# Kernel optimization log

Hardware: AMD Instinct MI355X
Metric: run time of the kernel (lower is better)

Reference implementation:

```python
import jax, jax.numpy as jnp
import numpy as np

NEG_SLOPE = 0.2  # PyG GATConv default leaky_relu slope
NUM_GRAPHS = 64


def gat_layer(x, src, dst, W, a_src, a_dst, b, heads, out_ch, concat, N):
    # x: [N, in_ch] -> h: [N, H, C]
    h = (x @ W).reshape(N, heads, out_ch)
    a_s = jnp.einsum('nhc,hc->nh', h, a_src)  # [N, H]
    a_d = jnp.einsum('nhc,hc->nh', h, a_dst)  # [N, H]
    e = jax.nn.leaky_relu(a_s[src] + a_d[dst], NEG_SLOPE)  # [E, H]
    # segment softmax over edges grouped by destination node
    emax = jax.ops.segment_max(e, dst, num_segments=N)
    emax = jnp.where(jnp.isfinite(emax), emax, 0.0)
    ex = jnp.exp(e - emax[dst])
    denom = jax.ops.segment_sum(ex, dst, num_segments=N)
    alpha = ex / (denom[dst] + 1e-16)  # [E, H]
    out = jax.ops.segment_sum(alpha[:, :, None] * h[src], dst, num_segments=N)  # [N, H, C]
    out = out.reshape(N, heads * out_ch) if concat else out.mean(axis=1)
    return out + b


def setup_inputs() -> dict:
    key = jax.random.key(0)
    ks = jax.random.split(key, 16)
    N, E, F_IN, H, C, NC = 50000, 800000, 128, 4, 64, 200
    x = jax.random.normal(ks[0], (N, F_IN), dtype=jnp.float32)
    edge_index = jax.random.randint(ks[1], (2, E), 0, N, dtype=jnp.int32)
    batch = jnp.sort(jax.random.randint(ks[2], (N,), 0, NUM_GRAPHS, dtype=jnp.int32))
    s = 0.05
    params = dict(
        W1=jax.random.normal(ks[3], (F_IN, H * C), jnp.float32) * s,
        a_src1=jax.random.normal(ks[4], (H, C), jnp.float32) * s,
        a_dst1=jax.random.normal(ks[5], (H, C), jnp.float32) * s,
        b1=jnp.zeros((H * C,), jnp.float32),
        W2=jax.random.normal(ks[6], (H * C, H * C), jnp.float32) * s,
        a_src2=jax.random.normal(ks[7], (H, C), jnp.float32) * s,
        a_dst2=jax.random.normal(ks[8], (H, C), jnp.float32) * s,
        b2=jnp.zeros((H * C,), jnp.float32),
        W3=jax.random.normal(ks[9], (H * C, C), jnp.float32) * s,
        a_src3=jax.random.normal(ks[10], (1, C), jnp.float32) * s,
        a_dst3=jax.random.normal(ks[11], (1, C), jnp.float32) * s,
        b3=jnp.zeros((C,), jnp.float32),
        Wc=jax.random.normal(ks[12], (C, NC), jnp.float32) * s,
        bc=jnp.zeros((NC,), jnp.float32),
    )
    return dict(x=x, edge_index=edge_index, batch=batch, **params)


def reference(x, edge_index, batch,
              W1, a_src1, a_dst1, b1,
              W2, a_src2, a_dst2, b2,
              W3, a_src3, a_dst3, b3,
              Wc, bc):
    N = x.shape[0]
    # PyG GATConv adds self-loops by default
    loop = jnp.arange(N, dtype=edge_index.dtype)
    src = jnp.concatenate([edge_index[0], loop])
    dst = jnp.concatenate([edge_index[1], loop])
    H, C = a_src1.shape
    h = gat_layer(x, src, dst, W1, a_src1, a_dst1, b1, H, C, True, N)
    h = jax.nn.elu(h)  # dropout is identity in eval mode
    h = gat_layer(h, src, dst, W2, a_src2, a_dst2, b2, H, C, True, N)
    h = jax.nn.elu(h)
    h = gat_layer(h, src, dst, W3, a_src3, a_dst3, b3, 1, C, False, N)
    h = jax.nn.elu(h)
    # global mean pool per graph
    sums = jax.ops.segment_sum(h, batch, num_segments=NUM_GRAPHS)
    counts = jax.ops.segment_sum(jnp.ones((N,), h.dtype), batch, num_segments=NUM_GRAPHS)
    pooled = sums / jnp.maximum(counts, 1.0)[:, None]
    return pooled @ Wc + bc
```

## Files before the change

### kernel.cpp

```cpp
#include <hip/hip_runtime.h>


typedef __attribute__((ext_vector_type(8))) __bf16 bf16x8;
typedef __attribute__((ext_vector_type(4))) float f32x4;
typedef __attribute__((ext_vector_type(8))) unsigned short u16x8;
typedef __attribute__((ext_vector_type(4))) unsigned short u16x4;

#define LOG2E 1.44269504f

static __device__ __forceinline__ unsigned short f2bf(float f) {
    unsigned u = __float_as_uint(f);
    unsigned r = (u + 0x7fffu + ((u >> 16) & 1u)) >> 16;
    return (unsigned short)r;
}
static __device__ __forceinline__ float bf2f(unsigned short s) {
    return __uint_as_float(((unsigned)s) << 16);
}

static __device__ __forceinline__ void g2lds16(const unsigned short* g,
                                               unsigned short* l) {
    __builtin_amdgcn_global_load_lds(
        (const __attribute__((address_space(1))) unsigned int*)g,
        (__attribute__((address_space(3))) unsigned int*)l, 16, 0, 0);
}

__global__ void count_edges(const int* __restrict__ ei, int* __restrict__ deg,
                            int* __restrict__ epos, int E) {
    int i = blockIdx.x * blockDim.x + threadIdx.x;
    if (i >= E) return;
    int dst = ei[E + i];
    epos[i] = atomicAdd(&deg[dst], 1);
}

__global__ __launch_bounds__(256) void scan_partial(const int* __restrict__ deg,
                                                    int* __restrict__ rowptr,
                                                    int* __restrict__ blockSums, int N) {
    int t = threadIdx.x;
    int lane = t & 63, wv = t >> 6;
    int base = blockIdx.x * 1024 + t * 4;
    int v[4];
#pragma unroll
    for (int j = 0; j < 4; ++j) v[j] = (base + j < N) ? deg[base + j] + 1 : 0;
    int local = v[0] + v[1] + v[2] + v[3];
    int x = local;
#pragma unroll
    for (int off = 1; off < 64; off <<= 1) {
        int y = __shfl_up(x, off);
        if (lane >= off) x += y;
    }
    __shared__ int wsum[4];
    if (lane == 63) wsum[wv] = x;
    __syncthreads();
    int woff = 0;
    for (int i = 0; i < wv; ++i) woff += wsum[i];
    int run = woff + x - local;
#pragma unroll
    for (int j = 0; j < 4; ++j) {
        if (base + j < N) rowptr[base + j] = run;
        run += v[j];
    }
    if (t == 255) blockSums[blockIdx.x] = woff + x;
}

__global__ void scan_blocks(int* __restrict__ blockSums, int* __restrict__ rowptr,
                            int NB, int N) {
    int lane = threadIdx.x;
    int carry = 0;
    for (int b0 = 0; b0 < NB; b0 += 64) {
        int i = b0 + lane;
        int v = (i < NB) ? blockSums[i] : 0;
        int x = v;
#pragma unroll
        for (int off = 1; off < 64; off <<= 1) {
            int y = __shfl_up(x, off);
            if (lane >= off) x += y;
        }
        if (i < NB) blockSums[i] = carry + x - v;
        carry += __shfl(x, 63);
    }
    if (lane == 0) {
        int c = N >> 10;
        int offN;
        if (c < NB) {
            offN = blockSums[c];
        } else {
            blockSums[c] = 0;
            offN = 0;
        }
        rowptr[N] = carry - offN;
    }
}

__global__ void scatter_edges(const int* __restrict__ ei, const int* __restrict__ rowptr,
                              const int* __restrict__ bs,
                              const int* __restrict__ deg, const int* __restrict__ epos,
                              int* __restrict__ srcs, int E, int N) {
    int i = blockIdx.x * blockDim.x + threadIdx.x;
    int tot = E + N;
    if (i >= tot) return;
    if (i < E) {
        int dst = ei[E + i];
        srcs[rowptr[dst] + bs[dst >> 10] + epos[i]] = ei[i];
    } else {
        int d = i - E;
        srcs[rowptr[d] + bs[d >> 10] + deg[d]] = d;
    }
}

__global__ void prep_cast(const float* __restrict__ W1, unsigned short* __restrict__ Wt1,
                          const float* __restrict__ W2, unsigned short* __restrict__ Wt2,
                          const float* __restrict__ W3, unsigned short* __restrict__ Wt3,
                          int n1, int n2, int n3, int F_IN, int HC, int C) {
    int i = blockIdx.x * blockDim.x + threadIdx.x;
    if (i < n1) {
        int n = i / F_IN, k = i - n * F_IN;
        Wt1[i] = f2bf(W1[(size_t)k * HC + n]);
        return;
    }
    i -= n1;
    if (i < n2) {
        int n = i / HC, k = i - n * HC;
        Wt2[i] = f2bf(W2[(size_t)k * HC + n]);
        return;
    }
    i -= n2;
    if (i < n3) {
        int n = i / HC, k = i - n * HC;
        Wt3[i] = f2bf(W3[(size_t)k * C + n]);
    }
}

#define BK 32

template <bool AF32, int WAVES_N>
__global__ __launch_bounds__(256) void gemm_bf16(const void* __restrict__ Av,
                                                 const unsigned short* __restrict__ Bt,
                                                 unsigned short* __restrict__ C,
                                                 const float* __restrict__ a_src,
                                                 const float* __restrict__ a_dst,
                                                 float* __restrict__ as_o,
                                                 float* __restrict__ ad_o,
                                                 int M, int N, int K, int H) {
    constexpr int BMt = (4 / WAVES_N) * 64;
    constexpr int BNt = WAVES_N * 64;
    constexpr int ASLOTS = BMt * 4;
    constexpr int ROUNDS = (BMt + BNt) / 64;
    __shared__ unsigned short As[BMt * BK];
    __shared__ unsigned short Bs[BNt * BK];
    int t = threadIdx.x;
    int bm = blockIdx.y * BMt;
    int wave = t >> 6, lane = t & 63;
    int wm = (wave / WAVES_N) * 64, wn = (wave % WAVES_N) * 64;
    int quad = lane >> 4, mr = lane & 15;

    f32x4 zero = {0.f, 0.f, 0.f, 0.f};
    f32x4 acc[4][4];
#pragma unroll
    for (int i = 0; i < 4; ++i)
#pragma unroll
        for (int j = 0; j < 4; ++j) acc[i][j] = zero;

    int sw = quad ^ ((mr >> 1) & 3);
    int aoff[4], boff[4];
#pragma unroll
    for (int i = 0; i < 4; ++i) {
        aoff[i] = (wm + i * 16 + mr) * BK + sw * 8;
        boff[i] = (wn + i * 16 + mr) * BK + sw * 8;
    }

    for (int k0 = 0; k0 < K; k0 += BK) {
        ushort4 ua0, ua1;
        if (AF32) {
            int slot = t;
            int row = slot >> 2;
            int sg = (slot & 3) ^ ((row >> 1) & 3);
            int gra = bm + row;
            float4 lo = make_float4(0.f, 0.f, 0.f, 0.f), hi = lo;
            if (gra < M) {
                const float* Af = (const float*)Av;
                lo = *(const float4*)&Af[(size_t)gra * K + k0 + sg * 8];
                hi = *(const float4*)&Af[(size_t)gra * K + k0 + sg * 8 + 4];
            }
            ua0 = make_ushort4(f2bf(lo.x), f2bf(lo.y), f2bf(lo.z), f2bf(lo.w));
            ua1 = make_ushort4(f2bf(hi.x), f2bf(hi.y), f2bf(hi.z), f2bf(hi.w));
        }
        __syncthreads();
        if (AF32) {
            int slot = t;
            *(ushort4*)&As[slot * 8]     = ua0;
            *(ushort4*)&As[slot * 8 + 4] = ua1;
#pragma unroll
            for (int r = 0; r < BNt / 64; ++r) {
                int slotw = r * 256 + wave * 64;
                int bslot = slotw + lane;
                int row = bslot >> 2;
                int sg = (bslot & 3) ^ ((row >> 1) & 3);
                g2lds16(&Bt[(size_t)row * K + k0 + sg * 8], &Bs[slotw * 8]);
            }
        } else {
            const unsigned short* Ab = (const unsigned short*)Av;
#pragma unroll
            for (int r = 0; r < ROUNDS; ++r) {
                int slotw = r * 256 + wave * 64;
                int slot = slotw + lane;
                if (slotw < ASLOTS) {
                    int row = slot >> 2;
                    int sg = (slot & 3) ^ ((row >> 1) & 3);
                    int gra = bm + row;
                    if (gra < M)
                        g2lds16(&Ab[(size_t)gra * K + k0 + sg * 8], &As[slotw * 8]);
                } else {
                    int bslot = slot - ASLOTS;
                    int row = bslot >> 2;
                    int sg = (bslot & 3) ^ ((row >> 1) & 3);
                    g2lds16(&Bt[(size_t)row * K + k0 + sg * 8], &Bs[(slotw - ASLOTS) * 8]);
                }
            }
        }
        __syncthreads();

        bf16x8 af[4], bfr[4];
#pragma unroll
        for (int i = 0; i < 4; ++i) {
            af[i]  = *(bf16x8*)&As[aoff[i]];
            bfr[i] = *(bf16x8*)&Bs[boff[i]];
        }
#pragma unroll
        for (int i = 0; i < 4; ++i)
#pragma unroll
            for (int j = 0; j < 4; ++j)
                acc[i][j] = __builtin_amdgcn_mfma_f32_16x16x32_bf16(af[i], bfr[j], acc[i][j], 0, 0, 0);
    }

    {
        int head = wn >> 6;
        float asv[4], adv[4];
#pragma unroll
        for (int j = 0; j < 4; ++j) {
            asv[j] = a_src[head * 64 + j * 16 + mr];
            adv[j] = a_dst[head * 64 + j * 16 + mr];
        }
#pragma unroll
        for (int i = 0; i < 4; ++i) {
#pragma unroll
            for (int r = 0; r < 4; ++r) {
                float ps = acc[i][0][r] * asv[0] + acc[i][1][r] * asv[1]
                         + acc[i][2][r] * asv[2] + acc[i][3][r] * asv[3];
                float pd = acc[i][0][r] * adv[0] + acc[i][1][r] * adv[1]
                         + acc[i][2][r] * adv[2] + acc[i][3][r] * adv[3];
#pragma unroll
                for (int off2 = 1; off2 < 16; off2 <<= 1) {
                    ps += __shfl_xor(ps, off2);
                    pd += __shfl_xor(pd, off2);
                }
                int grow = bm + wm + i * 16 + quad * 4 + r;
                if (mr == 0 && grow < M) {
                    as_o[(size_t)grow * H + head] = ps * LOG2E;
                    ad_o[(size_t)grow * H + head] = pd * LOG2E;
                }
            }
        }
    }

#pragma unroll
    for (int i = 0; i < 4; ++i) {
#pragma unroll
        for (int r = 0; r < 4; ++r) {
            int grow = bm + wm + i * 16 + quad * 4 + r;
            if (grow >= M) continue;
#pragma unroll
            for (int j = 0; j < 4; ++j) {
                int gcol = wn + j * 16 + mr;
                C[(size_t)grow * N + gcol] = f2bf(acc[i][j][r]);
            }
        }
    }
}

template <int H, int NPW, int VPL, bool OUTF32>
__global__ __launch_bounds__(256) void gat_aggregate(const unsigned short* __restrict__ hbuf,
                                                     const float* __restrict__ as_i,
                                                     const float* __restrict__ ad_i,
                                                     const int* __restrict__ rowptr,
                                                     const int* __restrict__ bs,
                                                     const int* __restrict__ srcs,
                                                     const float* __restrict__ bias,
                                                     void* __restrict__ out_v, int N) {
    constexpr int LPN = 64 / NPW;
    constexpr int HC = LPN * VPL;
    int wid = (blockIdx.x * blockDim.x + threadIdx.x) >> 6;
    int lane = threadIdx.x & 63;
    int sub = lane / LPN;
    int li  = lane % LPN;
    int node = wid * NPW + sub;
    if (node >= N) return;
    int row = rowptr[node] + bs[node >> 10];
    int end = rowptr[node + 1] + bs[(node + 1) >> 10];
    int len = end - row;
    const int hd_lane = (li * VPL) >> 6;

    float advh = ad_i[(size_t)node * H + hd_lane];

    float acc[VPL];
#pragma unroll
    for (int j = 0; j < VPL; ++j) acc[j] = 0.f;
    float l = 0.f;

    const int U = 4;
    for (int base = 0; base < len; base += U) {
        int s[U];
        float cf[U];
#pragma unroll
        for (int u = 0; u < U; ++u) {
            int idx = base + u;
            int ii = row + ((idx < len) ? idx : (len - 1));
            s[u] = srcs[ii];
        }
#pragma unroll
        for (int u = 0; u < U; ++u) cf[u] = as_i[(size_t)s[u] * H + hd_lane];
        if (VPL == 8) {
            u16x8 r[U];
#pragma unroll
            for (int u = 0; u < U; ++u)
                r[u] = *(const u16x8*)&hbuf[(size_t)s[u] * HC + li * VPL];
#pragma unroll
            for (int u = 0; u < U; ++u) {
                float e = cf[u] + advh;
                e = fmaxf(e, 0.2f * e);
                float wgt = (base + u < len) ? exp2f(e) : 0.f;
                l += wgt;
#pragma unroll
                for (int j = 0; j < 8; ++j) acc[j] += wgt * bf2f(r[u][j]);
            }
        } else {
            u16x4 r[U];
#pragma unroll
            for (int u = 0; u < U; ++u)
                r[u] = *(const u16x4*)&hbuf[(size_t)s[u] * HC + li * VPL];
#pragma unroll
            for (int u = 0; u < U; ++u) {
                float e = cf[u] + advh;
                e = fmaxf(e, 0.2f * e);
                float wgt = (base + u < len) ? exp2f(e) : 0.f;
                l += wgt;
#pragma unroll
                for (int j = 0; j < VPL; ++j) acc[j] += wgt * bf2f(r[u][j]);
            }
        }
    }

    float inv_l = 1.f / (l + 1e-16f);
    float vals[VPL];
#pragma unroll
    for (int j = 0; j < VPL; ++j) {
        float v = acc[j] * inv_l + bias[li * VPL + j];
        vals[j] = (v > 0.f) ? v : (__expf(v) - 1.f);
    }
    if (OUTF32) {
        float* out = (float*)out_v;
        if (VPL == 4) {
            float4 o = make_float4(vals[0], vals[1], vals[2], vals[3]);
            *(float4*)&out[(size_t)node * HC + li * 4] = o;
        } else {
#pragma unroll
            for (int j = 0; j < VPL; ++j)
                out[(size_t)node * HC + li * VPL + j] = vals[j];
        }
    } else {
        unsigned short* out = (unsigned short*)out_v;
        if (VPL == 8) {
            u16x8 o;
#pragma unroll
            for (int j = 0; j < 8; ++j) o[j] = f2bf(vals[j]);
            *(u16x8*)&out[(size_t)node * HC + li * 8] = o;
        } else {
            ushort4 o;
            o.x = f2bf(vals[0]); o.y = f2bf(vals[1]);
            o.z = f2bf(vals[2]); o.w = f2bf(vals[3]);
            *(ushort4*)&out[(size_t)node * HC + li * 4] = o;
        }
    }
}

#define POOL_CHUNK 128
__global__ __launch_bounds__(256) void pool_kernel(const float* __restrict__ hf,
                                                   const int* __restrict__ batch,
                                                   float* __restrict__ sums,
                                                   float* __restrict__ counts, int N) {
    int t = threadIdx.x;
    int c = t & 63, sub = t >> 6;
    int start = blockIdx.x * POOL_CHUNK;
    int end = min(start + POOL_CHUNK, N);
    float acc = 0.f, cnt = 0.f;
    int cur = -1;
    for (int n = start + sub; n < end; n += 4) {
        int g = batch[n];
        if (g != cur) {
            if (cur >= 0) {
                atomicAdd(&sums[cur * 64 + c], acc);
                if (c == 0) atomicAdd(&counts[cur], cnt);
            }
            cur = g; acc = 0.f; cnt = 0.f;
        }
        acc += hf[(size_t)n * 64 + c];
        cnt += 1.f;
    }
    if (cur >= 0) {
        atomicAdd(&sums[cur * 64 + c], acc);
        if (c == 0) atomicAdd(&counts[cur], cnt);
    }
}

__global__ void classify(const float* __restrict__ sums, const float* __restrict__ counts,
                         const float* __restrict__ Wc, const float* __restrict__ bc,
                         float* __restrict__ out, int NC) {
    __shared__ float p[64];
    int g = blockIdx.x;
    if (threadIdx.x < 64) {
        float cnt = fmaxf(counts[g], 1.0f);
        p[threadIdx.x] = sums[g * 64 + threadIdx.x] / cnt;
    }
    __syncthreads();
    int k = threadIdx.x;
    if (k < NC) {
        float acc = bc[k];
        for (int c = 0; c < 64; ++c) acc += p[c] * Wc[c * NC + k];
        out[g * NC + k] = acc;
    }
}

static inline size_t align_up(size_t x, size_t a) { return (x + a - 1) / a * a; }

extern "C" void kernel_launch(void* const* d_in, const int* in_sizes, int n_in,
                              void* d_out, int out_size, void* d_ws, size_t ws_size,
                              hipStream_t stream) {
    const float* x      = (const float*)d_in[0];
    const int*   ei     = (const int*)d_in[1];
    const int*   batch  = (const int*)d_in[2];
    const float* W1     = (const float*)d_in[3];
    const float* a_src1 = (const float*)d_in[4];
    const float* a_dst1 = (const float*)d_in[5];
    const float* b1     = (const float*)d_in[6];
    const float* W2     = (const float*)d_in[7];
    const float* a_src2 = (const float*)d_in[8];
    const float* a_dst2 = (const float*)d_in[9];
    const float* b2     = (const float*)d_in[10];
    const float* W3     = (const float*)d_in[11];
    const float* a_src3 = (const float*)d_in[12];
    const float* a_dst3 = (const float*)d_in[13];
    const float* b3     = (const float*)d_in[14];
    const float* Wc     = (const float*)d_in[15];
    const float* bc     = (const float*)d_in[16];

    const int N    = in_sizes[2];
    const int E    = in_sizes[1] / 2;
    const int F_IN = in_sizes[0] / N;
    const int HC   = in_sizes[6];
    const int C    = in_sizes[14];
    const int NC   = in_sizes[16];
    const int Etot = E + N;
    const int NB   = (N + 1023) / 1024;
    const int NPB  = (N + POOL_CHUNK - 1) / POOL_CHUNK;

    char* w = (char*)d_ws;
    size_t off = 0;
    auto alloc = [&](size_t bytes) -> void* {
        void* p = w + off;
        off = align_up(off + bytes, 256);
        return p;
    };
    int*   deg    = (int*)alloc((size_t)N * 4);
    float* sums   = (float*)alloc((size_t)(64 * 64 + 64) * 4);
    float* counts = sums + 64 * 64;
    int*   rowptr = (int*)alloc((size_t)(N + 1) * 4);
    int*   epos   = (int*)alloc((size_t)E * 4);
    int*   srcs   = (int*)alloc((size_t)Etot * 4);
    int*   bsums  = (int*)alloc((size_t)(NB + 1) * 4);
    float* as_buf = (float*)alloc((size_t)N * 4 * 4);
    float* ad_buf = (float*)alloc((size_t)N * 4 * 4);
    unsigned short* Wt1 = (unsigned short*)alloc((size_t)HC * F_IN * 2);
    unsigned short* Wt2 = (unsigned short*)alloc((size_t)HC * HC * 2);
    unsigned short* Wt3 = (unsigned short*)alloc((size_t)C * HC * 2);
    unsigned short* hA  = (unsigned short*)alloc((size_t)N * HC * 2);
    unsigned short* hB  = (unsigned short*)alloc((size_t)N * HC * 2);
    unsigned short* hC  = (unsigned short*)alloc((size_t)N * C * 2);
    float* bufF   = (float*)alloc((size_t)N * C * 4);

    const int TPB = 256;

    hipMemsetAsync(deg, 0, (char*)(sums + 64 * 64 + 64) - (char*)deg, stream);

    count_edges<<<(E + TPB - 1) / TPB, TPB, 0, stream>>>(ei, deg, epos, E);
    scan_partial<<<NB, 256, 0, stream>>>(deg, rowptr, bsums, N);
    scan_blocks<<<1, 64, 0, stream>>>(bsums, rowptr, NB, N);
    scatter_edges<<<(Etot + TPB - 1) / TPB, TPB, 0, stream>>>(ei, rowptr, bsums, deg, epos, srcs, E, N);

    int n1 = HC * F_IN, n2 = HC * HC, n3 = C * HC;
    int ntot = n1 + n2 + n3;
    prep_cast<<<(ntot + TPB - 1) / TPB, TPB, 0, stream>>>(
        W1, Wt1, W2, Wt2, W3, Wt3, n1, n2, n3, F_IN, HC, C);

    dim3 gWide(1, (N + 63) / 64);
    dim3 gNarrow(1, (N + 255) / 256);
    int aggBlocks12 = (((N + 1) / 2) + 3) / 4;
    int aggBlocks3  = (((N + 3) / 4) + 3) / 4;

    gemm_bf16<true, 4><<<gWide, 256, 0, stream>>>(x, Wt1, hA, a_src1, a_dst1, as_buf, ad_buf, N, HC, F_IN, 4);
    gat_aggregate<4, 2, 8, false><<<aggBlocks12, 256, 0, stream>>>(hA, as_buf, ad_buf, rowptr, bsums, srcs, b1, hB, N);

    gemm_bf16<false, 4><<<gWide, 256, 0, stream>>>(hB, Wt2, hA, a_src2, a_dst2, as_buf, ad_buf, N, HC, HC, 4);
    gat_aggregate<4, 2, 8, false><<<aggBlocks12, 256, 0, stream>>>(hA, as_buf, ad_buf, rowptr, bsums, srcs, b2, hB, N);

    gemm_bf16<false, 1><<<gNarrow, 256, 0, stream>>>(hB, Wt3, hC, a_src3, a_dst3, as_buf, ad_buf, N, C, HC, 1);
    gat_aggregate<1, 4, 4, true><<<aggBlocks3, 256, 0, stream>>>(hC, as_buf, ad_buf, rowptr, bsums, srcs, b3, bufF, N);

    pool_kernel<<<NPB, 256, 0, stream>>>(bufF, batch, sums, counts, N);
    classify<<<64, 256, 0, stream>>>(sums, counts, Wc, bc, (float*)d_out, NC);
}
```

Baseline: 399.8 us.

## Cooperatively load edge indices and double-buffer gathers in GAT aggregation

Each lane now loads one source index per chunk of LPN edges, and the indices are spread across the node's lanes with shuffles, so serial scalar index loads are no longer needed. The gather loop is software-pipelined with two register buffers: the next group of attention scalars and feature vectors is issued before the current group is accumulated, which hides memory latency. This raises register pressure and may issue extra clamped or wasted loads past the end of each chunk.

```diff
diff --git a/kernel.cpp b/kernel.cpp
--- a/kernel.cpp
+++ b/kernel.cpp
@@ -277,6 +277,10 @@
     }
 }
 
+template <int VPL> struct VecT;
+template <> struct VecT<8> { using T = u16x8; };
+template <> struct VecT<4> { using T = u16x4; };
+
 template <int H, int NPW, int VPL, bool OUTF32>
 __global__ __launch_bounds__(256) void gat_aggregate(const unsigned short* __restrict__ hbuf,
                                                      const float* __restrict__ as_i,
@@ -288,6 +292,8 @@
                                                      void* __restrict__ out_v, int N) {
     constexpr int LPN = 64 / NPW;
     constexpr int HC = LPN * VPL;
+    constexpr int U = 4;
+    using vload = typename VecT<VPL>::T;
     int wid = (blockIdx.x * blockDim.x + threadIdx.x) >> 6;
     int lane = threadIdx.x & 63;
     int sub = lane / LPN;
@@ -298,55 +304,70 @@
     int end = rowptr[node + 1] + bs[(node + 1) >> 10];
     int len = end - row;
     const int hd_lane = (li * VPL) >> 6;
+    const int subbase = sub * LPN;
 
     float advh = ad_i[(size_t)node * H + hd_lane];
+    const unsigned short* hb_l = hbuf + li * VPL;
 
     float acc[VPL];
 #pragma unroll
     for (int j = 0; j < VPL; ++j) acc[j] = 0.f;
     float l = 0.f;
 
-    const int U = 4;
-    for (int base = 0; base < len; base += U) {
-        int s[U];
-        float cf[U];
-#pragma unroll
-        for (int u = 0; u < U; ++u) {
-            int idx = base + u;
-            int ii = row + ((idx < len) ? idx : (len - 1));
-            s[u] = srcs[ii];
-        }
-#pragma unroll
-        for (int u = 0; u < U; ++u) cf[u] = as_i[(size_t)s[u] * H + hd_lane];
-        if (VPL == 8) {
-            u16x8 r[U];
-#pragma unroll
-            for (int u = 0; u < U; ++u)
-                r[u] = *(const u16x8*)&hbuf[(size_t)s[u] * HC + li * VPL];
-#pragma unroll
-            for (int u = 0; u < U; ++u) {
-                float e = cf[u] + advh;
-                e = fmaxf(e, 0.2f * e);
-                float wgt = (base + u < len) ? exp2f(e) : 0.f;
-                l += wgt;
-#pragma unroll
-                for (int j = 0; j < 8; ++j) acc[j] += wgt * bf2f(r[u][j]);
-            }
-        } else {
-            u16x4 r[U];
-#pragma unroll
-            for (int u = 0; u < U; ++u)
-                r[u] = *(const u16x4*)&hbuf[(size_t)s[u] * HC + li * VPL];
-#pragma unroll
-            for (int u = 0; u < U; ++u) {
-                float e = cf[u] + advh;
-                e = fmaxf(e, 0.2f * e);
-                float wgt = (base + u < len) ? exp2f(e) : 0.f;
-                l += wgt;
-#pragma unroll
-                for (int j = 0; j < VPL; ++j) acc[j] += wgt * bf2f(r[u][j]);
-            }
-        }
+    for (int c0 = 0; c0 < len; c0 += LPN) {
+        int cend = len - c0; cend = (cend < LPN) ? cend : LPN;
+        if (cend <= 0) break;
+        int ei_ = c0 + li; ei_ = (ei_ < len) ? ei_ : (len - 1);
+        int svec = srcs[row + ei_];
+
+        int sA[U], sB[U];
+        float cfA[U], cfB[U];
+        vload rA[U], rB[U];
+
+#define AGG_ISSUE(sX, cfX, rX, b0)                                          \
+        do {                                                                \
+            _Pragma("unroll")                                               \
+            for (int u = 0; u < U; ++u) {                                   \
+                int idx = (b0) + u;                                         \
+                idx = (idx < cend) ? idx : (cend - 1);                      \
+                sX[u] = __shfl(svec, subbase + idx);                        \
+            }                                                               \
+            _Pragma("unroll")                                               \
+            for (int u = 0; u < U; ++u)                                     \
+                cfX[u] = as_i[(size_t)sX[u] * H + hd_lane];                 \
+            _Pragma("unroll")                                               \
+            for (int u = 0; u < U; ++u)                                     \
+                rX[u] = *(const vload*)&hb_l[(size_t)sX[u] * HC];           \
+        } while (0)
+
+#define AGG_COMPUTE(cfX, rX, b0)                                            \
+        do {                                                                \
+            _Pragma("unroll")                                               \
+            for (int u = 0; u < U; ++u) {                                   \
+                float e = cfX[u] + advh;                                    \
+                e = fmaxf(e, 0.2f * e);                                     \
+                float wgt = ((b0) + u < cend) ? exp2f(e) : 0.f;             \
+                l += wgt;                                                   \
+                _Pragma("unroll")                                           \
+                for (int j = 0; j < VPL; ++j)                               \
+                    acc[j] += wgt * bf2f(rX[u][j]);                         \
+            }                                                               \
+        } while (0)
+
+        AGG_ISSUE(sA, cfA, rA, 0);
+        int b = 0;
+        while (true) {
+            AGG_ISSUE(sB, cfB, rB, b + U);
+            AGG_COMPUTE(cfA, rA, b);
+            b += U;
+            if (b >= cend) break;
+            AGG_ISSUE(sA, cfA, rA, b + U);
+            AGG_COMPUTE(cfB, rB, b);
+            b += U;
+            if (b >= cend) break;
+        }
+#undef AGG_ISSUE
+#undef AGG_COMPUTE
     }
 
     float inv_l = 1.f / (l + 1e-16f);
```

Result: no change. 406.3 us (+1.6%).

## Fold attention vectors into weights, double-buffer GEMM LDS, unroll aggregation more

Applied to the files above, without the earlier changes.

Precomputes W·a_src and W·a_dst as an extra 16-column bf16 matrix so the attention logits come from an extra MFMA per k-step instead of a shuffle reduction in the epilogue. Double-buffers the A/B/W LDS tiles so global loads for the next k-tile overlap the MFMAs on the current one, at the cost of doubled shared memory. Raises the edge unroll in the aggregation kernel from 4 to 8 for more memory-level parallelism. The attention logits now use bf16-rounded folded weights, which changes precision slightly.

```diff
diff --git a/kernel.cpp b/kernel.cpp
--- a/kernel.cpp
+++ b/kernel.cpp
@@ -4,7 +4,6 @@
 typedef __attribute__((ext_vector_type(8))) __bf16 bf16x8;
 typedef __attribute__((ext_vector_type(4))) float f32x4;
 typedef __attribute__((ext_vector_type(8))) unsigned short u16x8;
-typedef __attribute__((ext_vector_type(4))) unsigned short u16x4;
 
 #define LOG2E 1.44269504f
 
@@ -130,14 +129,61 @@
     }
 }
 
+__global__ void prep_asd(const float* __restrict__ W1, const float* __restrict__ as1,
+                         const float* __restrict__ ad1,
+                         const float* __restrict__ W2, const float* __restrict__ as2,
+                         const float* __restrict__ ad2,
+                         const float* __restrict__ W3, const float* __restrict__ as3,
+                         const float* __restrict__ ad3,
+                         unsigned short* __restrict__ wasd1,
+                         unsigned short* __restrict__ wasd2,
+                         unsigned short* __restrict__ wasd3) {
+    int i = blockIdx.x * blockDim.x + threadIdx.x;
+    if (i < 16 * 128) {
+        int p = i >> 7, k = i & 127;
+        float v = 0.f;
+        if (p < 8) {
+            const float* a = (p < 4) ? as1 : ad1;
+            int hh = p & 3;
+            for (int c = 0; c < 64; ++c)
+                v += W1[(size_t)k * 256 + hh * 64 + c] * a[hh * 64 + c];
+        }
+        wasd1[i] = f2bf(v);
+        return;
+    }
+    i -= 16 * 128;
+    if (i < 16 * 256) {
+        int p = i >> 8, k = i & 255;
+        float v = 0.f;
+        if (p < 8) {
+            const float* a = (p < 4) ? as2 : ad2;
+            int hh = p & 3;
+            for (int c = 0; c < 64; ++c)
+                v += W2[(size_t)k * 256 + hh * 64 + c] * a[hh * 64 + c];
+        }
+        wasd2[i] = f2bf(v);
+        return;
+    }
+    i -= 16 * 256;
+    if (i < 16 * 256) {
+        int p = i >> 8, k = i & 255;
+        float v = 0.f;
+        if (p < 2) {
+            const float* a = p ? ad3 : as3;
+            for (int c = 0; c < 64; ++c)
+                v += W3[(size_t)k * 64 + c] * a[c];
+        }
+        wasd3[i] = f2bf(v);
+    }
+}
+
 #define BK 32
 
 template <bool AF32, int WAVES_N>
 __global__ __launch_bounds__(256) void gemm_bf16(const void* __restrict__ Av,
                                                  const unsigned short* __restrict__ Bt,
+                                                 const unsigned short* __restrict__ Wasd,
                                                  unsigned short* __restrict__ C,
-                                                 const float* __restrict__ a_src,
-                                                 const float* __restrict__ a_dst,
                                                  float* __restrict__ as_o,
                                                  float* __restrict__ ad_o,
                                                  int M, int N, int K, int H) {
@@ -145,8 +191,10 @@
     constexpr int BNt = WAVES_N * 64;
     constexpr int ASLOTS = BMt * 4;
     constexpr int ROUNDS = (BMt + BNt) / 64;
-    __shared__ unsigned short As[BMt * BK];
-    __shared__ unsigned short Bs[BNt * BK];
+    constexpr bool ASD_ALL = (WAVES_N == 1);
+    __shared__ unsigned short As[2][BMt * BK];
+    __shared__ unsigned short Bs[2][BNt * BK];
+    __shared__ unsigned short Ws[2][16 * BK];
     int t = threadIdx.x;
     int bm = blockIdx.y * BMt;
     int wave = t >> 6, lane = t & 63;
@@ -159,6 +207,9 @@
     for (int i = 0; i < 4; ++i)
 #pragma unroll
         for (int j = 0; j < 4; ++j) acc[i][j] = zero;
+    f32x4 acc4[4];
+#pragma unroll
+    for (int i = 0; i < 4; ++i) acc4[i] = zero;
 
     int sw = quad ^ ((mr >> 1) & 3);
     int aoff[4], boff[4];
@@ -168,98 +219,115 @@
         boff[i] = (wn + i * 16 + mr) * BK + sw * 8;
     }
 
-    for (int k0 = 0; k0 < K; k0 += BK) {
-        ushort4 ua0, ua1;
-        if (AF32) {
-            int slot = t;
-            int row = slot >> 2;
-            int sg = (slot & 3) ^ ((row >> 1) & 3);
-            int gra = bm + row;
-            float4 lo = make_float4(0.f, 0.f, 0.f, 0.f), hi = lo;
-            if (gra < M) {
-                const float* Af = (const float*)Av;
-                lo = *(const float4*)&Af[(size_t)gra * K + k0 + sg * 8];
-                hi = *(const float4*)&Af[(size_t)gra * K + k0 + sg * 8 + 4];
-            }
-            ua0 = make_ushort4(f2bf(lo.x), f2bf(lo.y), f2bf(lo.z), f2bf(lo.w));
-            ua1 = make_ushort4(f2bf(hi.x), f2bf(hi.y), f2bf(hi.z), f2bf(hi.w));
-        }
-        __syncthreads();
-        if (AF32) {
-            int slot = t;
-            *(ushort4*)&As[slot * 8]     = ua0;
-            *(ushort4*)&As[slot * 8 + 4] = ua1;
-#pragma unroll
-            for (int r = 0; r < BNt / 64; ++r) {
-                int slotw = r * 256 + wave * 64;
-                int bslot = slotw + lane;
+    auto stage_ab = [&](int bsel, int kk) {
+        const unsigned short* Ab = (const unsigned short*)Av;
+#pragma unroll
+        for (int r = 0; r < ROUNDS; ++r) {
+            int slotw = r * 256 + wave * 64;
+            int slot = slotw + lane;
+            if (slotw < ASLOTS) {
+                int row = slot >> 2;
+                int sg = (slot & 3) ^ ((row >> 1) & 3);
+                int gra = bm + row;
+                if (gra < M)
+                    g2lds16(&Ab[(size_t)gra * K + kk + sg * 8], &As[bsel][slotw * 8]);
+            } else {
+                int bslot = slot - ASLOTS;
                 int row = bslot >> 2;
                 int sg = (bslot & 3) ^ ((row >> 1) & 3);
-                g2lds16(&Bt[(size_t)row * K + k0 + sg * 8], &Bs[slotw * 8]);
-            }
-        } else {
-            const unsigned short* Ab = (const unsigned short*)Av;
-#pragma unroll
-            for (int r = 0; r < ROUNDS; ++r) {
-                int slotw = r * 256 + wave * 64;
-                int slot = slotw + lane;
-                if (slotw < ASLOTS) {
-                    int row = slot >> 2;
-                    int sg = (slot & 3) ^ ((row >> 1) & 3);
-                    int gra = bm + row;
-                    if (gra < M)
-                        g2lds16(&Ab[(size_t)gra * K + k0 + sg * 8], &As[slotw * 8]);
-                } else {
-                    int bslot = slot - ASLOTS;
-                    int row = bslot >> 2;
-                    int sg = (bslot & 3) ^ ((row >> 1) & 3);
-                    g2lds16(&Bt[(size_t)row * K + k0 + sg * 8], &Bs[(slotw - ASLOTS) * 8]);
-                }
-            }
-        }
-        __syncthreads();
-
+                g2lds16(&Bt[(size_t)row * K + kk + sg * 8], &Bs[bsel][(slotw - ASLOTS) * 8]);
+            }
+        }
+        if (wave == 0)
+            g2lds16(&Wasd[(size_t)(lane >> 2) * K + kk + (lane & 3) * 8], &Ws[bsel][0]);
+    };
+    auto stage_b_af32 = [&](int bsel, int kk) {
+#pragma unroll
+        for (int r = 0; r < BNt / 64; ++r) {
+            int slotw = r * 256 + wave * 64;
+            int bslot = slotw + lane;
+            int row = bslot >> 2;
+            int sg = (bslot & 3) ^ ((row >> 1) & 3);
+            g2lds16(&Bt[(size_t)row * K + kk + sg * 8], &Bs[bsel][slotw * 8]);
+        }
+        if (wave == 0)
+            g2lds16(&Wasd[(size_t)(lane >> 2) * K + kk + (lane & 3) * 8], &Ws[bsel][0]);
+    };
+    auto loadA_f32 = [&](int kk, float4& lo, float4& hi) {
+        int slot = t, row = slot >> 2;
+        int sg = (slot & 3) ^ ((row >> 1) & 3);
+        int gra = bm + row;
+        lo = make_float4(0.f, 0.f, 0.f, 0.f); hi = lo;
+        if (gra < M) {
+            const float* Af = (const float*)Av;
+            lo = *(const float4*)&Af[(size_t)gra * K + kk + sg * 8];
+            hi = *(const float4*)&Af[(size_t)gra * K + kk + sg * 8 + 4];
+        }
+    };
+    auto writeA = [&](int bsel, float4 lo, float4 hi) {
+        int slot = t;
+        *(ushort4*)&As[bsel][slot * 8]     = make_ushort4(f2bf(lo.x), f2bf(lo.y), f2bf(lo.z), f2bf(lo.w));
+        *(ushort4*)&As[bsel][slot * 8 + 4] = make_ushort4(f2bf(hi.x), f2bf(hi.y), f2bf(hi.z), f2bf(hi.w));
+    };
+
+    const int nt = K / BK;
+    int cur = 0;
+
+    if (AF32) {
+        float4 l0, h0;
+        loadA_f32(0, l0, h0);
+        writeA(0, l0, h0);
+        stage_b_af32(0, 0);
+    } else {
+        stage_ab(0, 0);
+    }
+    __syncthreads();
+
+    for (int ts = 0; ts < nt; ++ts) {
+        int nxt = cur ^ 1;
+        bool more = (ts + 1 < nt);
+        float4 plo, phi;
+        if (more) {
+            if (AF32) {
+                loadA_f32((ts + 1) * BK, plo, phi);
+                stage_b_af32(nxt, (ts + 1) * BK);
+            } else {
+                stage_ab(nxt, (ts + 1) * BK);
+            }
+        }
         bf16x8 af[4], bfr[4];
 #pragma unroll
         for (int i = 0; i < 4; ++i) {
-            af[i]  = *(bf16x8*)&As[aoff[i]];
-            bfr[i] = *(bf16x8*)&Bs[boff[i]];
+            af[i]  = *(bf16x8*)&As[cur][aoff[i]];
+            bfr[i] = *(bf16x8*)&Bs[cur][boff[i]];
         }
 #pragma unroll
         for (int i = 0; i < 4; ++i)
 #pragma unroll
             for (int j = 0; j < 4; ++j)
                 acc[i][j] = __builtin_amdgcn_mfma_f32_16x16x32_bf16(af[i], bfr[j], acc[i][j], 0, 0, 0);
-    }
-
-    {
-        int head = wn >> 6;
-        float asv[4], adv[4];
-#pragma unroll
-        for (int j = 0; j < 4; ++j) {
-            asv[j] = a_src[head * 64 + j * 16 + mr];
-            adv[j] = a_dst[head * 64 + j * 16 + mr];
-        }
-#pragma unroll
-        for (int i = 0; i < 4; ++i) {
+        if (ASD_ALL || wave == 0) {
+            bf16x8 wsf = *(bf16x8*)&Ws[cur][mr * BK + quad * 8];
+#pragma unroll
+            for (int i = 0; i < 4; ++i)
+                acc4[i] = __builtin_amdgcn_mfma_f32_16x16x32_bf16(af[i], wsf, acc4[i], 0, 0, 0);
+        }
+        if (more && AF32) writeA(nxt, plo, phi);
+        __syncthreads();
+        cur = nxt;
+    }
+
+    if ((ASD_ALL || wave == 0) && mr < 2 * H) {
+#pragma unroll
+        for (int i = 0; i < 4; ++i)
 #pragma unroll
             for (int r = 0; r < 4; ++r) {
-                float ps = acc[i][0][r] * asv[0] + acc[i][1][r] * asv[1]
-                         + acc[i][2][r] * asv[2] + acc[i][3][r] * asv[3];
-                float pd = acc[i][0][r] * adv[0] + acc[i][1][r] * adv[1]
-                         + acc[i][2][r] * adv[2] + acc[i][3][r] * adv[3];
-#pragma unroll
-                for (int off2 = 1; off2 < 16; off2 <<= 1) {
-                    ps += __shfl_xor(ps, off2);
-                    pd += __shfl_xor(pd, off2);
-                }
                 int grow = bm + wm + i * 16 + quad * 4 + r;
-                if (mr == 0 && grow < M) {
-                    as_o[(size_t)grow * H + head] = ps * LOG2E;
-                    ad_o[(size_t)grow * H + head] = pd * LOG2E;
-                }
-            }
-        }
+                if (grow >= M) continue;
+                float v = acc4[i][r] * LOG2E;
+                if (mr < H) as_o[(size_t)grow * H + mr] = v;
+                else        ad_o[(size_t)grow * H + (mr - H)] = v;
+            }
     }
 
 #pragma unroll
@@ -306,7 +374,7 @@
     for (int j = 0; j < VPL; ++j) acc[j] = 0.f;
     float l = 0.f;
 
-    const int U = 4;
+    const int U = 8;
     for (int base = 0; base < len; base += U) {
         int s[U];
         float cf[U];
@@ -322,7 +390,7 @@
             u16x8 r[U];
 #pragma unroll
             for (int u = 0; u < U; ++u)
-                r[u] = *(const u16x8*)&hbuf[(size_t)s[u] * HC + li * VPL];
+                r[u] = *(const u16x8*)&hbuf[(size_t)s[u] * HC + li * 8];
 #pragma unroll
             for (int u = 0; u < U; ++u) {
                 float e = cf[u] + advh;
@@ -333,18 +401,20 @@
                 for (int j = 0; j < 8; ++j) acc[j] += wgt * bf2f(r[u][j]);
             }
         } else {
-            u16x4 r[U];
+            ushort4 r[U];
 #pragma unroll
             for (int u = 0; u < U; ++u)
-                r[u] = *(const u16x4*)&hbuf[(size_t)s[u] * HC + li * VPL];
+                r[u] = *(const ushort4*)&hbuf[(size_t)s[u] * HC + li * 4];
 #pragma unroll
             for (int u = 0; u < U; ++u) {
                 float e = cf[u] + advh;
                 e = fmaxf(e, 0.2f * e);
                 float wgt = (base + u < len) ? exp2f(e) : 0.f;
                 l += wgt;
-#pragma unroll
-                for (int j = 0; j < VPL; ++j) acc[j] += wgt * bf2f(r[u][j]);
+                acc[0] += wgt * bf2f(r[u].x);
+                acc[1] += wgt * bf2f(r[u].y);
+                acc[2] += wgt * bf2f(r[u].z);
+                acc[3] += wgt * bf2f(r[u].w);
             }
         }
     }
@@ -481,6 +551,9 @@
     unsigned short* Wt1 = (unsigned short*)alloc((size_t)HC * F_IN * 2);
     unsigned short* Wt2 = (unsigned short*)alloc((size_t)HC * HC * 2);
     unsigned short* Wt3 = (unsigned short*)alloc((size_t)C * HC * 2);
+    unsigned short* wasd1 = (unsigned short*)alloc((size_t)16 * F_IN * 2);
+    unsigned short* wasd2 = (unsigned short*)alloc((size_t)16 * HC * 2);
+    unsigned short* wasd3 = (unsigned short*)alloc((size_t)16 * HC * 2);
     unsigned short* hA  = (unsigned short*)alloc((size_t)N * HC * 2);
     unsigned short* hB  = (unsigned short*)alloc((size_t)N * HC * 2);
     unsigned short* hC  = (unsigned short*)alloc((size_t)N * C * 2);
@@ -499,19 +572,23 @@
     int ntot = n1 + n2 + n3;
     prep_cast<<<(ntot + TPB - 1) / TPB, TPB, 0, stream>>>(
         W1, Wt1, W2, Wt2, W3, Wt3, n1, n2, n3, F_IN, HC, C);
+    int nasd = 16 * F_IN + 16 * HC + 16 * HC;
+    prep_asd<<<(nasd + TPB - 1) / TPB, TPB, 0, stream>>>(
+        W1, a_src1, a_dst1, W2, a_src2, a_dst2, W3, a_src3, a_dst3,
+        wasd1, wasd2, wasd3);
 
     dim3 gWide(1, (N + 63) / 64);
     dim3 gNarrow(1, (N + 255) / 256);
     int aggBlocks12 = (((N + 1) / 2) + 3) / 4;
     int aggBlocks3  = (((N + 3) / 4) + 3) / 4;
 
-    gemm_bf16<true, 4><<<gWide, 256, 0, stream>>>(x, Wt1, hA, a_src1, a_dst1, as_buf, ad_buf, N, HC, F_IN, 4);
+    gemm_bf16<true, 4><<<gWide, 256, 0, stream>>>(x, Wt1, wasd1, hA, as_buf, ad_buf, N, HC, F_IN, 4);
     gat_aggregate<4, 2, 8, false><<<aggBlocks12, 256, 0, stream>>>(hA, as_buf, ad_buf, rowptr, bsums, srcs, b1, hB, N);
 
-    gemm_bf16<false, 4><<<gWide, 256, 0, stream>>>(hB, Wt2, hA, a_src2, a_dst2, as_buf, ad_buf, N, HC, HC, 4);
+    gemm_bf16<false, 4><<<gWide, 256, 0, stream>>>(hB, Wt2, wasd2, hA, as_buf, ad_buf, N, HC, HC, 4);
     gat_aggregate<4, 2, 8, false><<<aggBlocks12, 256, 0, stream>>>(hA, as_buf, ad_buf, rowptr, bsums, srcs, b2, hB, N);
 
-    gemm_bf16<false, 1><<<gNarrow, 256, 0, stream>>>(hB, Wt3, hC, a_src3, a_dst3, as_buf, ad_buf, N, C, HC, 1);
+    gemm_bf16<false, 1><<<gNarrow, 256, 0, stream>>>(hB, Wt3, wasd3, hC, as_buf, ad_buf, N, C, HC, 1);
     gat_aggregate<1, 4, 4, true><<<aggBlocks3, 256, 0, stream>>>(hC, as_buf, ad_buf, rowptr, bsums, srcs, b3, bufF, N);
 
     pool_kernel<<<NPB, 256, 0, stream>>>(bufF, batch, sums, counts, N);
```

Result: no change. 398.6 us (-0.3%).
